# Kernel optimization log

Measured on AMD Instinct MI355X. Metric: run time of the kernel, lower is better.

Reference implementation:

```python
import jax, jax.numpy as jnp
import numpy as np

QKV = 1024   # qkv_size (input feature dim)
E = 64       # embed_size (per-head dim)
H = 16       # num_heads
OUT = 1024   # output_size
B, S = 8, 1024


def setup_inputs() -> dict:
    key = jax.random.key(0)
    ks = jax.random.split(key, 8)
    inv = 1.0 / np.sqrt(QKV)
    return {
        "query": jax.random.normal(ks[0], (B, S, QKV), jnp.float32),
        "key": jax.random.normal(ks[1], (B, S, QKV), jnp.float32),
        "value": jax.random.normal(ks[2], (B, S, QKV), jnp.float32),
        # stacked per-head projection weights, torch Linear convention y = x @ W.T -> store as [H, QKV, E]
        "Wq": jax.random.normal(ks[3], (H, QKV, E), jnp.float32) * inv,
        "Wk": jax.random.normal(ks[4], (H, QKV, E), jnp.float32) * inv,
        "Wv": jax.random.normal(ks[5], (H, QKV, E), jnp.float32) * inv,
        "Wo": jax.random.normal(ks[6], (OUT, H * E), jnp.float32) / np.sqrt(H * E),
        "bo": jax.random.normal(ks[7], (OUT,), jnp.float32) * 0.01,
    }


def reference(query, key, value, Wq, Wk, Wv, Wo, bo):
    # batched over heads: [B,S,QKV] x [H,QKV,E] -> [B,H,S,E]
    Q = jnp.einsum("bsd,hde->bhse", query, Wq)
    K = jnp.einsum("bsd,hde->bhse", key, Wk)
    V = jnp.einsum("bsd,hde->bhse", value, Wv)
    # NOTE: original scales by sqrt(qkv_dim) (input dim), not per-head dim
    scale = 1.0 / jnp.sqrt(jnp.float32(QKV))
    scores = jnp.einsum("bhse,bhte->bhst", Q, K) * scale  # [B,H,S,S]
    attn = jax.nn.softmax(scores, axis=-1)
    attended = jnp.einsum("bhst,bhte->bhse", attn, V)     # [B,H,S,E]
    # concat heads along last dim (head-major order matches torch.cat of head outputs)
    concat = attended.transpose(0, 2, 1, 3).reshape(query.shape[0], query.shape[1], H * E)
    return concat @ Wo.T + bo
```

## Files before the change

### kernel.cpp

```cpp
#include <hip/hip_runtime.h>
#include <stdint.h>


typedef __bf16 bf16x8 __attribute__((ext_vector_type(8)));
typedef float f32x4 __attribute__((ext_vector_type(4)));

typedef __attribute__((address_space(3))) uint32_t lds_u32;
typedef const __attribute__((address_space(1))) uint32_t glb_u32;

__device__ __forceinline__ ushort f2bf(float f) {
  union { __bf16 b; ushort u; } c;
  c.b = (__bf16)f;
  return c.u;
}
__device__ __forceinline__ bf16x8 ld8(const ushort* p) {
  union { uint4 u; bf16x8 b; } c;
  c.u = *reinterpret_cast<const uint4*>(p);
  return c.b;
}
__device__ __forceinline__ void cvt16(const float* __restrict__ src,
                                      ushort* __restrict__ dst) {
  union { uint4 u[2]; ushort s[16]; } o;
#pragma unroll
  for (int i = 0; i < 4; ++i) {
    const float4 f = reinterpret_cast<const float4*>(src)[i];
    o.s[4 * i + 0] = f2bf(f.x);
    o.s[4 * i + 1] = f2bf(f.y);
    o.s[4 * i + 2] = f2bf(f.z);
    o.s[4 * i + 3] = f2bf(f.w);
  }
  reinterpret_cast<uint4*>(dst)[0] = o.u[0];
  reinterpret_cast<uint4*>(dst)[1] = o.u[1];
}

__device__ __forceinline__ void gld16(const ushort* g, ushort* l) {
  __builtin_amdgcn_global_load_lds((glb_u32*)g, (lds_u32*)l, 16, 0, 0);
}

__global__ __launch_bounds__(256) void prep_wt3(
    const float* __restrict__ W0, const float* __restrict__ W1,
    const float* __restrict__ W2, ushort* __restrict__ T0,
    ushort* __restrict__ T1, ushort* __restrict__ T2) {
  __shared__ __align__(16) ushort tile[64 * 72];
  const int sel = blockIdx.x >> 8;
  const float* W = sel == 0 ? W0 : sel == 1 ? W1 : W2;
  ushort* WT = sel == 0 ? T0 : sel == 1 ? T1 : T2;
  const int bid = blockIdx.x & 255;
  const int h = bid >> 4;
  const int kt = bid & 15;
  const int t = threadIdx.x;
  const int row = t >> 2;
  const int ch = (t & 3) * 16;
  cvt16(W + ((size_t)h * 1024 + kt * 64 + row) * 64 + ch, &tile[row * 72 + ch]);
  __syncthreads();
  const int e = t >> 2;
  const int kc = (t & 3) * 16;
  ushort vals[16];
#pragma unroll
  for (int j = 0; j < 16; ++j) vals[j] = tile[(kc + j) * 72 + e];
  ushort* dst = WT + (size_t)(h * 64 + e) * 1024 + kt * 64 + kc;
  reinterpret_cast<uint4*>(dst)[0] = *reinterpret_cast<uint4*>(&vals[0]);
  reinterpret_cast<uint4*>(dst)[1] = *reinterpret_cast<uint4*>(&vals[8]);
}

__global__ __launch_bounds__(256) void cvt3(const float* __restrict__ s0,
                                            ushort* __restrict__ d0,
                                            const float* __restrict__ s1,
                                            ushort* __restrict__ d1,
                                            const float* __restrict__ s2,
                                            ushort* __restrict__ d2) {
  int b = blockIdx.x;
  const float* s;
  ushort* d;
  if (b < 2048) { s = s0; d = d0; }
  else if (b < 4096) { s = s1; d = d1; b -= 2048; }
  else { s = s2; d = d2; b -= 4096; }
  const int i = (b * 256 + threadIdx.x) * 16;
  cvt16(s + i, d + i);
}

template <bool F32OUT, int BN>
__device__ __forceinline__ void core_bb_pipe(ushort* __restrict__ S,
                                             const ushort* __restrict__ A,
                                             const ushort* __restrict__ Bt,
                                             const float* __restrict__ bias,
                                             void* __restrict__ Cv,
                                             float oscale, int bx, int by) {
  constexpr int JN = BN / 32;
  constexpr int BLOADS = BN / 32;
  constexpr int WN = BN / 2;
  ushort* A0 = S;
  ushort* B0 = S + 128 * 64;
  ushort* A1 = S + 128 * 64 + BN * 64;
  ushort* B1 = S + 2 * 128 * 64 + BN * 64;
  const int n0 = bx * BN;
  const int m0 = by * 128;
  const int t = threadIdx.x;
  const int lane = t & 63;
  const int w = t >> 6;
  const int wm = w >> 1, wn = w & 1;
  const int col = lane & 15;
  const int quad = lane >> 4;
  const int gr = lane >> 3;
  const int gc = ((lane & 7) ^ gr) * 8;
  const int s7 = col & 7;

  f32x4 acc[4][JN];
#pragma unroll
  for (int i = 0; i < 4; ++i)
#pragma unroll
    for (int j = 0; j < JN; ++j) acc[i][j] = (f32x4){0.f, 0.f, 0.f, 0.f};

  const ushort* a_src = A + (size_t)(m0 + w * 8 + gr) * 1024 + gc;
  const ushort* b_src = Bt + (size_t)(n0 + w * 8 + gr) * 1024 + gc;

  auto stage = [&](ushort* as, ushort* bs, int k0) {
#pragma unroll
    for (int c = 0; c < 4; ++c)
      gld16(a_src + (size_t)c * 32 * 1024 + k0, as + (w * 8 + c * 32) * 64);
#pragma unroll
    for (int c = 0; c < BLOADS; ++c)
      gld16(b_src + (size_t)c * 32 * 1024 + k0, bs + (w * 8 + c * 32) * 64);
  };
  auto wait_prev = [&]() {
    if constexpr (BN == 128)
      asm volatile("s_waitcnt vmcnt(8)" ::: "memory");
    else
      asm volatile("s_waitcnt vmcnt(6)" ::: "memory");
  };

  auto compute = [&](const ushort* asb, const ushort* bsb) {
#pragma unroll
    for (int half = 0; half < 2; ++half) {
      bf16x8 af[4], bfr[JN];
      const int g0 = half * 4 + quad;
      const int gs = (g0 ^ s7) << 3;
#pragma unroll
      for (int i = 0; i < 4; ++i)
        af[i] = ld8(&asb[(wm * 64 + i * 16 + col) * 64 + gs]);
#pragma unroll
      for (int j = 0; j < JN; ++j)
        bfr[j] = ld8(&bsb[(wn * WN + j * 16 + col) * 64 + gs]);
#pragma unroll
      for (int i = 0; i < 4; ++i)
#pragma unroll
        for (int j = 0; j < JN; ++j)
          acc[i][j] = __builtin_amdgcn_mfma_f32_16x16x32_bf16(af[i], bfr[j],
                                                              acc[i][j], 0, 0, 0);
    }
  };

  stage(A0, B0, 0);

  for (int t2 = 0; t2 < 16; t2 += 2) {
    stage(A1, B1, (t2 + 1) * 64);
    wait_prev();
    __builtin_amdgcn_sched_barrier(0);
    __builtin_amdgcn_s_barrier();
    __builtin_amdgcn_sched_barrier(0);
    compute(A0, B0);
    asm volatile("s_waitcnt lgkmcnt(0)" ::: "memory");
    __builtin_amdgcn_sched_barrier(0);
    __builtin_amdgcn_s_barrier();

    if (t2 < 14) {
      stage(A0, B0, (t2 + 2) * 64);
      wait_prev();
    } else {
      asm volatile("s_waitcnt vmcnt(0)" ::: "memory");
    }
    __builtin_amdgcn_sched_barrier(0);
    __builtin_amdgcn_s_barrier();
    __builtin_amdgcn_sched_barrier(0);
    compute(A1, B1);
    asm volatile("s_waitcnt lgkmcnt(0)" ::: "memory");
    __builtin_amdgcn_sched_barrier(0);
    __builtin_amdgcn_s_barrier();
  }

#pragma unroll
  for (int i = 0; i < 4; ++i)
#pragma unroll
    for (int j = 0; j < JN; ++j) {
      const int n = n0 + wn * WN + j * 16 + col;
      float bv = 0.f;
      if (F32OUT) bv = bias[n];
#pragma unroll
      for (int r = 0; r < 4; ++r) {
        const int m = m0 + wm * 64 + i * 16 + quad * 4 + r;
        if (F32OUT)
          reinterpret_cast<float*>(Cv)[(size_t)m * 1024 + n] = acc[i][j][r] + bv;
        else
          reinterpret_cast<ushort*>(Cv)[(size_t)m * 1024 + n] =
              f2bf(acc[i][j][r] * oscale);
      }
    }
}

__device__ __forceinline__ void core_f32a(ushort* __restrict__ S,
                                          const float* __restrict__ A,
                                          const ushort* __restrict__ Bt,
                                          ushort* __restrict__ C, int bx,
                                          int by) {
  ushort* As72 = S;
  ushort* Bs = S + 128 * 72;
  const int n0 = bx * 128;
  const int m0 = by * 128;
  const int t = threadIdx.x;
  const int lane = t & 63;
  const int w = t >> 6;
  const int wm = w >> 1, wn = w & 1;
  const int col = lane & 15;
  const int quad = lane >> 4;
  const int gr = lane >> 3;
  const int gc = ((lane & 7) ^ gr) * 8;
  const int s7 = col & 7;
  const int srow = t >> 1;
  const int sc0 = (t & 1) * 32;

  f32x4 acc[4][4];
#pragma unroll
  for (int i = 0; i < 4; ++i)
#pragma unroll
    for (int j = 0; j < 4; ++j) acc[i][j] = (f32x4){0.f, 0.f, 0.f, 0.f};

  const float* a_src = A + (size_t)(m0 + srow) * 1024 + sc0;
  const ushort* b_src = Bt + (size_t)(n0 + w * 8 + gr) * 1024 + gc;
  ushort* bs_base = &Bs[(w * 8) * 64];

  for (int k0 = 0; k0 < 1024; k0 += 64) {
#pragma unroll
    for (int c = 0; c < 4; ++c)
      gld16(b_src + (size_t)c * 32 * 1024 + k0, bs_base + c * 32 * 64);
    cvt16(a_src + k0, &As72[srow * 72 + sc0]);
    cvt16(a_src + k0 + 16, &As72[srow * 72 + sc0 + 16]);
    __syncthreads();

#pragma unroll
    for (int half = 0; half < 2; ++half) {
      bf16x8 af[4], bfr[4];
      const int gs = ((half * 4 + quad) ^ s7) << 3;
#pragma unroll
      for (int i = 0; i < 4; ++i)
        af[i] = ld8(&As72[(wm * 64 + i * 16 + col) * 72 + half * 32 + quad * 8]);
#pragma unroll
      for (int j = 0; j < 4; ++j)
        bfr[j] = ld8(&Bs[(wn * 64 + j * 16 + col) * 64 + gs]);
#pragma unroll
      for (int i = 0; i < 4; ++i)
#pragma unroll
        for (int j = 0; j < 4; ++j)
          acc[i][j] = __builtin_amdgcn_mfma_f32_16x16x32_bf16(af[i], bfr[j],
                                                              acc[i][j], 0, 0, 0);
    }
    __syncthreads();
  }

#pragma unroll
  for (int i = 0; i < 4; ++i)
#pragma unroll
    for (int j = 0; j < 4; ++j) {
      const int n = n0 + wn * 64 + j * 16 + col;
#pragma unroll
      for (int r = 0; r < 4; ++r) {
        const int m = m0 + wm * 64 + i * 16 + quad * 4 + r;
        C[(size_t)m * 1024 + n] = f2bf(acc[i][j][r]);
      }
    }
}

__global__ __launch_bounds__(256) void gemm_out(const ushort* __restrict__ A,
                                                const ushort* __restrict__ Bt,
                                                const float* __restrict__ bias,
                                                float* __restrict__ C) {
  __shared__ __align__(16) ushort S[2 * 128 * 64 + 2 * 64 * 64];
  const int id = blockIdx.x;
  const int bx = (id >> 3) & 15;
  const int by = ((id >> 7) << 3) | (id & 7);
  core_bb_pipe<true, 64>(S, A, Bt, bias, C, 1.0f, bx, by);
}

__global__ __launch_bounds__(256) void gemm_proj3(
    const ushort* __restrict__ Aq, const ushort* __restrict__ Bq,
    ushort* __restrict__ Cq, const ushort* __restrict__ Ak,
    const ushort* __restrict__ Bk, ushort* __restrict__ Ck,
    const float* __restrict__ Av, const ushort* __restrict__ Bv,
    ushort* __restrict__ Cvp) {
  __shared__ __align__(16) ushort S[4 * 128 * 64];
  const int id = blockIdx.x;
  const int bx = (id >> 3) & 7;
  const int by = ((id >> 6) << 3) | (id & 7);
  if (by < 64)
    core_bb_pipe<false, 128>(S, Aq, Bq, nullptr, Cq, 0.03125f, bx, by);
  else if (by < 128)
    core_bb_pipe<false, 128>(S, Ak, Bk, nullptr, Ck, 1.0f, bx, by - 64);
  else
    core_f32a(S, Av, Bv, Cvp, bx, by - 128);
}

__global__ __launch_bounds__(256) void flash_attn(const ushort* __restrict__ Q,
                                                  const ushort* __restrict__ K,
                                                  const ushort* __restrict__ V,
                                                  ushort* __restrict__ O) {
  __shared__ __align__(16) ushort QP[128 * 72];
  __shared__ __align__(16) ushort Ks[64 * 64];
  __shared__ __align__(16) ushort Vt[64 * 72];
  const int pair = blockIdx.x & 127;
  const int b = pair >> 4;
  const int h = pair & 15;
  const int qt = blockIdx.x >> 7;
  const int t = threadIdx.x;
  const int lane = t & 63;
  const int w = t >> 6;
  const int col = lane & 15;
  const int quad = lane >> 4;

  const size_t base = (size_t)b * 1024 * 1024 + h * 64;
  const int qrow0 = qt * 128;

  {
    const int row = t >> 1;
    const int c0 = (t & 1) * 32;
    const ushort* src = Q + base + (size_t)(qrow0 + row) * 1024 + c0;
    uint4 v0 = reinterpret_cast<const uint4*>(src)[0];
    uint4 v1 = reinterpret_cast<const uint4*>(src)[1];
    uint4 v2 = reinterpret_cast<const uint4*>(src)[2];
    uint4 v3 = reinterpret_cast<const uint4*>(src)[3];
    reinterpret_cast<uint4*>(&QP[row * 72 + c0])[0] = v0;
    reinterpret_cast<uint4*>(&QP[row * 72 + c0])[1] = v1;
    reinterpret_cast<uint4*>(&QP[row * 72 + c0])[2] = v2;
    reinterpret_cast<uint4*>(&QP[row * 72 + c0])[3] = v3;
  }
  __syncthreads();
  bf16x8 qa[2][2];
#pragma unroll
  for (int g = 0; g < 2; ++g)
#pragma unroll
    for (int half = 0; half < 2; ++half)
      qa[g][half] =
          ld8(&QP[(w * 32 + g * 16 + col) * 72 + half * 32 + quad * 8]);

  f32x4 o_[2][4];
#pragma unroll
  for (int g = 0; g < 2; ++g)
#pragma unroll
    for (int c = 0; c < 4; ++c) o_[g][c] = (f32x4){0.f, 0.f, 0.f, 0.f};
  float m_s[2] = {-1e30f, -1e30f};
  float l_s[2] = {0.f, 0.f};

  const int krow = w * 16 + (lane >> 3);
  const int kcs = (((lane & 7) ^ (lane >> 3)) << 3);
  const int s7 = col & 7;

  for (int kt = 0; kt < 16; ++kt) {
    {
      const ushort* k0 = K + base + (size_t)(kt * 64 + krow) * 1024 + kcs;
      gld16(k0, &Ks[(w * 16) * 64]);
      gld16(k0 + 8 * 1024, &Ks[(w * 16 + 8) * 64]);
      const int vs = t & 63;
      const int ve = (t >> 6) * 16;
      const ushort* vsrc = V + base + (size_t)(kt * 64 + vs) * 1024 + ve;
      union { uint4 u[2]; ushort s[16]; } vv;
      vv.u[0] = reinterpret_cast<const uint4*>(vsrc)[0];
      vv.u[1] = reinterpret_cast<const uint4*>(vsrc)[1];
#pragma unroll
      for (int j = 0; j < 16; ++j) Vt[(ve + j) * 72 + vs] = vv.s[j];
    }
    __syncthreads();

    f32x4 sc[2][4];
    __builtin_amdgcn_s_setprio(1);
#pragma unroll
    for (int c = 0; c < 4; ++c) {
      const int R = (c * 16 + col) * 64;
      bf16x8 kb0 = ld8(&Ks[R + ((quad ^ s7) << 3)]);
      bf16x8 kb1 = ld8(&Ks[R + (((quad + 4) ^ s7) << 3)]);
#pragma unroll
      for (int g = 0; g < 2; ++g) {
        f32x4 z = {0.f, 0.f, 0.f, 0.f};
        z = __builtin_amdgcn_mfma_f32_16x16x32_bf16(kb0, qa[g][0], z, 0, 0, 0);
        z = __builtin_amdgcn_mfma_f32_16x16x32_bf16(kb1, qa[g][1], z, 0, 0, 0);
        sc[g][c] = z;
      }
    }
    __builtin_amdgcn_s_setprio(0);

    float al[2];
    bool df[2];
#pragma unroll
    for (int g = 0; g < 2; ++g) {
      float mx = sc[g][0][0];
#pragma unroll
      for (int c = 0; c < 4; ++c)
#pragma unroll
        for (int r = 0; r < 4; ++r) mx = fmaxf(mx, sc[g][c][r]);
      mx = fmaxf(mx, __shfl_xor(mx, 16));
      mx = fmaxf(mx, __shfl_xor(mx, 32));
      df[g] = __all(mx - m_s[g] <= 8.0f) != 0;
      if (df[g]) {
        al[g] = 1.0f;
      } else {
        const float m_new = fmaxf(m_s[g], mx);
        al[g] = __expf(m_s[g] - m_new);
        m_s[g] = m_new;
      }
      float rs = 0.f;
      const int prow = (w * 32 + g * 16 + col) * 72;
#pragma unroll
      for (int c = 0; c < 4; ++c) {
        const float p0 = __expf(sc[g][c][0] - m_s[g]);
        const float p1 = __expf(sc[g][c][1] - m_s[g]);
        const float p2 = __expf(sc[g][c][2] - m_s[g]);
        const float p3 = __expf(sc[g][c][3] - m_s[g]);
        rs += (p0 + p1) + (p2 + p3);
        union { uint2 u; ushort s[4]; } pk;
        pk.s[0] = f2bf(p0);
        pk.s[1] = f2bf(p1);
        pk.s[2] = f2bf(p2);
        pk.s[3] = f2bf(p3);
        *reinterpret_cast<uint2*>(&QP[prow + c * 16 + quad * 4]) = pk.u;
      }
      rs += __shfl_xor(rs, 16);
      rs += __shfl_xor(rs, 32);
      l_s[g] = df[g] ? (l_s[g] + rs) : (l_s[g] * al[g] + rs);
    }

#pragma unroll
    for (int g = 0; g < 2; ++g)
      if (!df[g]) {
#pragma unroll
        for (int r = 0; r < 4; ++r) {
          const float a = __shfl(al[g], (lane & 48) | (quad * 4 + r));
          o_[g][0][r] *= a;
          o_[g][1][r] *= a;
          o_[g][2][r] *= a;
          o_[g][3][r] *= a;
        }
      }

    bf16x8 pa[2][2];
#pragma unroll
    for (int g = 0; g < 2; ++g)
#pragma unroll
      for (int half = 0; half < 2; ++half)
        pa[g][half] =
            ld8(&QP[(w * 32 + g * 16 + col) * 72 + half * 32 + quad * 8]);
    __builtin_amdgcn_s_setprio(1);
#pragma unroll
    for (int c = 0; c < 4; ++c) {
      bf16x8 vb0 = ld8(&Vt[(c * 16 + col) * 72 + quad * 8]);
      bf16x8 vb1 = ld8(&Vt[(c * 16 + col) * 72 + 32 + quad * 8]);
#pragma unroll
      for (int g = 0; g < 2; ++g) {
        o_[g][c] = __builtin_amdgcn_mfma_f32_16x16x32_bf16(pa[g][0], vb0,
                                                           o_[g][c], 0, 0, 0);
        o_[g][c] = __builtin_amdgcn_mfma_f32_16x16x32_bf16(pa[g][1], vb1,
                                                           o_[g][c], 0, 0, 0);
      }
    }
    __builtin_amdgcn_s_setprio(0);
    __syncthreads();
  }

#pragma unroll
  for (int g = 0; g < 2; ++g)
#pragma unroll
    for (int r = 0; r < 4; ++r) {
      const float lr = __shfl(l_s[g], (lane & 48) | (quad * 4 + r));
      const float inv = 1.f / lr;
      const size_t row =
          base + (size_t)(qrow0 + w * 32 + g * 16 + quad * 4 + r) * 1024;
      O[row + 0 + col] = f2bf(o_[g][0][r] * inv);
      O[row + 16 + col] = f2bf(o_[g][1][r] * inv);
      O[row + 32 + col] = f2bf(o_[g][2][r] * inv);
      O[row + 48 + col] = f2bf(o_[g][3][r] * inv);
    }
}

extern "C" void kernel_launch(void* const* d_in, const int* in_sizes, int n_in,
                              void* d_out, int out_size, void* d_ws, size_t ws_size,
                              hipStream_t stream) {
  const float* q = (const float*)d_in[0];
  const float* k = (const float*)d_in[1];
  const float* v = (const float*)d_in[2];
  const float* Wq = (const float*)d_in[3];
  const float* Wk = (const float*)d_in[4];
  const float* Wv = (const float*)d_in[5];
  const float* Wo = (const float*)d_in[6];
  const float* bo = (const float*)d_in[7];
  float* out = (float*)d_out;
  ushort* ws = (ushort*)d_ws;

  const size_t M8 = 8u << 20;
  const size_t M1 = 1u << 20;
  ushort* Qp = ws;
  ushort* Kp = ws + M8;
  ushort* Vp = ws + 2 * M8;
  ushort* WqT = ws + 3 * M8;
  ushort* WkT = WqT + M1;
  ushort* WvT = WkT + M1;
  ushort* WoB = WvT + M1;

  ushort* X0 = (ushort*)d_out;
  ushort* X1 = X0 + M8;

  prep_wt3<<<768, 256, 0, stream>>>(Wq, Wk, Wv, WqT, WkT, WvT);
  cvt3<<<4352, 256, 0, stream>>>(q, X0, k, X1, Wo, WoB);
  gemm_proj3<<<1536, 256, 0, stream>>>(X0, WqT, Qp, X1, WkT, Kp, v, WvT, Vp);

  flash_attn<<<1024, 256, 0, stream>>>(Qp, Kp, Vp, Qp);

  gemm_out<<<1024, 256, 0, stream>>>(Qp, WoB, bo, out);
}
```

Measured before the change: 322.3 us.

## Store V projection transposed and double-buffer K/V tiles in flash attention

The V projection epilogue now writes its output transposed ([H*E, B*S]) with packed 4-element stores, so flash attention can load V tiles with direct async global-to-LDS copies instead of a register transpose into LDS. The attention loop is restructured to double-buffer K and V in LDS, prefetching the next tile while computing the current one, with explicit waitcnt and barriers. This is meant to hide global load latency and remove the scalar LDS transpose stores. In exchange it uses more LDS, which could lower occupancy, and the transposed stores from the projection GEMM are strided.

```diff
diff --git a/kernel.cpp b/kernel.cpp
--- a/kernel.cpp
+++ b/kernel.cpp
@@ -197,11 +197,11 @@
     }
 }
 
-__device__ __forceinline__ void core_f32a(ushort* __restrict__ S,
-                                          const float* __restrict__ A,
-                                          const ushort* __restrict__ Bt,
-                                          ushort* __restrict__ C, int bx,
-                                          int by) {
+__device__ __forceinline__ void core_f32a_T(ushort* __restrict__ S,
+                                            const float* __restrict__ A,
+                                            const ushort* __restrict__ Bt,
+                                            ushort* __restrict__ Ct, int bx,
+                                            int by) {
   ushort* As72 = S;
   ushort* Bs = S + 128 * 72;
   const int n0 = bx * 128;
@@ -261,11 +261,11 @@
 #pragma unroll
     for (int j = 0; j < 4; ++j) {
       const int n = n0 + wn * 64 + j * 16 + col;
-#pragma unroll
-      for (int r = 0; r < 4; ++r) {
-        const int m = m0 + wm * 64 + i * 16 + quad * 4 + r;
-        C[(size_t)m * 1024 + n] = f2bf(acc[i][j][r]);
-      }
+      const int mb = m0 + wm * 64 + i * 16 + quad * 4;
+      union { uint2 u; ushort s[4]; } pk;
+#pragma unroll
+      for (int r = 0; r < 4; ++r) pk.s[r] = f2bf(acc[i][j][r]);
+      *reinterpret_cast<uint2*>(&Ct[(size_t)n * 8192 + mb]) = pk.u;
     }
 }
 
@@ -285,7 +285,7 @@
     ushort* __restrict__ Cq, const ushort* __restrict__ Ak,
     const ushort* __restrict__ Bk, ushort* __restrict__ Ck,
     const float* __restrict__ Av, const ushort* __restrict__ Bv,
-    ushort* __restrict__ Cvp) {
+    ushort* __restrict__ Cvt) {
   __shared__ __align__(16) ushort S[4 * 128 * 64];
   const int id = blockIdx.x;
   const int bx = (id >> 3) & 7;
@@ -295,16 +295,18 @@
   else if (by < 128)
     core_bb_pipe<false, 128>(S, Ak, Bk, nullptr, Ck, 1.0f, bx, by - 64);
   else
-    core_f32a(S, Av, Bv, Cvp, bx, by - 128);
+    core_f32a_T(S, Av, Bv, Cvt, bx, by - 128);
 }
 
 __global__ __launch_bounds__(256) void flash_attn(const ushort* __restrict__ Q,
                                                   const ushort* __restrict__ K,
-                                                  const ushort* __restrict__ V,
+                                                  const ushort* __restrict__ VT,
                                                   ushort* __restrict__ O) {
   __shared__ __align__(16) ushort QP[128 * 72];
-  __shared__ __align__(16) ushort Ks[64 * 64];
-  __shared__ __align__(16) ushort Vt[64 * 72];
+  __shared__ __align__(16) ushort Ks0[64 * 64];
+  __shared__ __align__(16) ushort Ks1[64 * 64];
+  __shared__ __align__(16) ushort Vt0[64 * 64];
+  __shared__ __align__(16) ushort Vt1[64 * 64];
   const int pair = blockIdx.x & 127;
   const int b = pair >> 4;
   const int h = pair & 15;
@@ -348,33 +350,30 @@
   float m_s[2] = {-1e30f, -1e30f};
   float l_s[2] = {0.f, 0.f};
 
-  const int krow = w * 16 + (lane >> 3);
-  const int kcs = (((lane & 7) ^ (lane >> 3)) << 3);
+  const int gr = lane >> 3;
+  const int kcs = (((lane & 7) ^ gr) << 3);
   const int s7 = col & 7;
-
-  for (int kt = 0; kt < 16; ++kt) {
-    {
-      const ushort* k0 = K + base + (size_t)(kt * 64 + krow) * 1024 + kcs;
-      gld16(k0, &Ks[(w * 16) * 64]);
-      gld16(k0 + 8 * 1024, &Ks[(w * 16 + 8) * 64]);
-      const int vs = t & 63;
-      const int ve = (t >> 6) * 16;
-      const ushort* vsrc = V + base + (size_t)(kt * 64 + vs) * 1024 + ve;
-      union { uint4 u[2]; ushort s[16]; } vv;
-      vv.u[0] = reinterpret_cast<const uint4*>(vsrc)[0];
-      vv.u[1] = reinterpret_cast<const uint4*>(vsrc)[1];
-#pragma unroll
-      for (int j = 0; j < 16; ++j) Vt[(ve + j) * 72 + vs] = vv.s[j];
-    }
-    __syncthreads();
-
+  const ushort* krowp = K + base + (size_t)(w * 16 + gr) * 1024 + kcs;
+  const ushort* vrowp =
+      VT + (size_t)(h * 64 + w * 16 + gr) * 8192 + (size_t)b * 1024 + kcs;
+
+  auto stageKV = [&](ushort* kb, ushort* vb, int kt) {
+    const ushort* k0 = krowp + (size_t)kt * 64 * 1024;
+    gld16(k0, kb + (w * 16) * 64);
+    gld16(k0 + (size_t)8 * 1024, kb + (w * 16 + 8) * 64);
+    const ushort* v0 = vrowp + kt * 64;
+    gld16(v0, vb + (w * 16) * 64);
+    gld16(v0 + (size_t)8 * 8192, vb + (w * 16 + 8) * 64);
+  };
+
+  auto body = [&](const ushort* kb, const ushort* vb) {
     f32x4 sc[2][4];
     __builtin_amdgcn_s_setprio(1);
 #pragma unroll
     for (int c = 0; c < 4; ++c) {
       const int R = (c * 16 + col) * 64;
-      bf16x8 kb0 = ld8(&Ks[R + ((quad ^ s7) << 3)]);
-      bf16x8 kb1 = ld8(&Ks[R + (((quad + 4) ^ s7) << 3)]);
+      bf16x8 kb0 = ld8(&kb[R + ((quad ^ s7) << 3)]);
+      bf16x8 kb1 = ld8(&kb[R + (((quad + 4) ^ s7) << 3)]);
 #pragma unroll
       for (int g = 0; g < 2; ++g) {
         f32x4 z = {0.f, 0.f, 0.f, 0.f};
@@ -448,8 +447,9 @@
     __builtin_amdgcn_s_setprio(1);
 #pragma unroll
     for (int c = 0; c < 4; ++c) {
-      bf16x8 vb0 = ld8(&Vt[(c * 16 + col) * 72 + quad * 8]);
-      bf16x8 vb1 = ld8(&Vt[(c * 16 + col) * 72 + 32 + quad * 8]);
+      const int R = (c * 16 + col) * 64;
+      bf16x8 vb0 = ld8(&vb[R + ((quad ^ s7) << 3)]);
+      bf16x8 vb1 = ld8(&vb[R + (((quad + 4) ^ s7) << 3)]);
 #pragma unroll
       for (int g = 0; g < 2; ++g) {
         o_[g][c] = __builtin_amdgcn_mfma_f32_16x16x32_bf16(pa[g][0], vb0,
@@ -459,7 +459,35 @@
       }
     }
     __builtin_amdgcn_s_setprio(0);
-    __syncthreads();
+  };
+
+  stageKV(Ks0, Vt0, 0);
+  __syncthreads();
+
+  for (int t2 = 0; t2 < 16; t2 += 2) {
+    stageKV(Ks1, Vt1, t2 + 1);
+    asm volatile("s_waitcnt vmcnt(4)" ::: "memory");
+    __builtin_amdgcn_sched_barrier(0);
+    __builtin_amdgcn_s_barrier();
+    __builtin_amdgcn_sched_barrier(0);
+    body(Ks0, Vt0);
+    asm volatile("s_waitcnt lgkmcnt(0)" ::: "memory");
+    __builtin_amdgcn_sched_barrier(0);
+    __builtin_amdgcn_s_barrier();
+
+    if (t2 < 14) {
+      stageKV(Ks0, Vt0, t2 + 2);
+      asm volatile("s_waitcnt vmcnt(4)" ::: "memory");
+    } else {
+      asm volatile("s_waitcnt vmcnt(0)" ::: "memory");
+    }
+    __builtin_amdgcn_sched_barrier(0);
+    __builtin_amdgcn_s_barrier();
+    __builtin_amdgcn_sched_barrier(0);
+    body(Ks1, Vt1);
+    asm volatile("s_waitcnt lgkmcnt(0)" ::: "memory");
+    __builtin_amdgcn_sched_barrier(0);
+    __builtin_amdgcn_s_barrier();
   }
 
 #pragma unroll
@@ -495,7 +523,7 @@
   const size_t M1 = 1u << 20;
   ushort* Qp = ws;
   ushort* Kp = ws + M8;
-  ushort* Vp = ws + 2 * M8;
+  ushort* VpT = ws + 2 * M8;
   ushort* WqT = ws + 3 * M8;
   ushort* WkT = WqT + M1;
   ushort* WvT = WkT + M1;
@@ -506,9 +534,9 @@
 
   prep_wt3<<<768, 256, 0, stream>>>(Wq, Wk, Wv, WqT, WkT, WvT);
   cvt3<<<4352, 256, 0, stream>>>(q, X0, k, X1, Wo, WoB);
-  gemm_proj3<<<1536, 256, 0, stream>>>(X0, WqT, Qp, X1, WkT, Kp, v, WvT, Vp);
-
-  flash_attn<<<1024, 256, 0, stream>>>(Qp, Kp, Vp, Qp);
+  gemm_proj3<<<1536, 256, 0, stream>>>(X0, WqT, Qp, X1, WkT, Kp, v, WvT, VpT);
+
+  flash_attn<<<1024, 256, 0, stream>>>(Qp, Kp, VpT, Qp);
 
   gemm_out<<<1024, 256, 0, stream>>>(Qp, WoB, bo, out);
 }
```

Result: faster. 312.6 us (-3.0%).
